# Performance work log

Measured on AMD Instinct MI355X. Metric: run time of the kernel, lower is better.

The kernel has to match this reference:

```python
import jax, jax.numpy as jnp
import numpy as np

V = 9488  # vocab_size + 1
H = 512   # rnn_size = att_hid_size = input_encoding_size
F = 2048  # fc/att feat size

def setup_inputs() -> dict:
    key = jax.random.key(0)
    ks = jax.random.split(key, 16)
    s = 0.02
    return {
        'fc_feats': jax.random.normal(ks[0], (64, F), jnp.float32),
        'att_feats': jax.random.normal(ks[1], (64, 196, F), jnp.float32),
        'seq': jax.random.randint(ks[2], (64, 17), 0, 9487),
        'lin_W': jax.random.normal(ks[3], (H, F), jnp.float32) * s,
        'lin_b': jnp.zeros((H,), jnp.float32),
        'emb': jax.random.uniform(ks[4], (V, H), jnp.float32, -0.1, 0.1),
        'Wih': jax.random.normal(ks[5], (4 * H, H + F), jnp.float32) * s,
        'Whh': jax.random.normal(ks[6], (4 * H, H), jnp.float32) * s,
        'ctx_W': jax.random.normal(ks[7], (H, F), jnp.float32) * s,
        'ctx_b': jnp.zeros((H,), jnp.float32),
        'h2a_W': jax.random.normal(ks[8], (H, H), jnp.float32) * s,
        'h2a_b': jnp.zeros((H,), jnp.float32),
        'alpha_W': jax.random.normal(ks[9], (1, H), jnp.float32) * s,
        'alpha_b': jnp.zeros((1,), jnp.float32),
        'logit_W': jax.random.uniform(ks[10], (V, H), jnp.float32, -0.1, 0.1),
        'logit_b': jnp.zeros((V,), jnp.float32),
    }

def reference(fc_feats, att_feats, seq, lin_W, lin_b, emb, Wih, Whh,
              ctx_W, ctx_b, h2a_W, h2a_b, alpha_W, alpha_b, logit_W, logit_b):
    # init_hidden: h0 = c0 = Linear(fc_feats)  -> [B, H]
    h0 = fc_feats @ lin_W.T + lin_b
    # ctx2att(att_feats) is constant across timesteps -> compute once. [B, L, H]
    p_att = jnp.einsum('blf,hf->blh', att_feats, ctx_W) + ctx_b
    tokens = seq[:, :-1].T  # [T-1, B]

    def step(carry, it):
        h, c = carry
        xt = emb[it]                                   # [B, H]
        att_h = h @ h2a_W.T + h2a_b                    # [B, H]
        dot = jnp.tanh(p_att + att_h[:, None, :])      # [B, L, H]
        e = jnp.einsum('blh,h->bl', dot, alpha_W[0]) + alpha_b[0]
        w = jax.nn.softmax(e, axis=-1)                 # [B, L]
        att_res = jnp.einsum('bl,blf->bf', w, att_feats)  # [B, F]
        x = jnp.concatenate([xt, att_res], axis=1)     # [B, H+F]
        gates = x @ Wih.T + h @ Whh.T                  # bias=False LSTM
        i_g, f_g, g_g, o_g = jnp.split(gates, 4, axis=1)  # torch order i,f,g,o
        c_n = jax.nn.sigmoid(f_g) * c + jax.nn.sigmoid(i_g) * jnp.tanh(g_g)
        h_n = jax.nn.sigmoid(o_g) * jnp.tanh(c_n)
        logp = jax.nn.log_softmax(h_n @ logit_W.T + logit_b, axis=-1)
        return (h_n, c_n), logp

    _, outs = jax.lax.scan(step, (h0, h0), tokens)     # [T-1, B, V]
    return jnp.transpose(outs, (1, 0, 2))              # [B, T-1, V]
```

## Files before the change

### kernel.cpp

```cpp
#include <hip/hip_runtime.h>
#include <stdint.h>
#include <stddef.h>

#define BB 64
#define LL 196
#define FF 2048
#define HH 512
#define VV 9488
#define NPAD 9600
#define TT 16
#define KXX 3072
#define MM (BB * LL)

typedef short short8 __attribute__((ext_vector_type(8)));
typedef short short4v __attribute__((ext_vector_type(4)));
typedef float f32x4 __attribute__((ext_vector_type(4)));
typedef unsigned short u16;
typedef unsigned char u8;

typedef __attribute__((address_space(3))) uint32_t lds_u32_t;
typedef __attribute__((address_space(1))) const uint32_t glb_u32_t;

__device__ __forceinline__ u16 f2bf(float f) {
  uint32_t u = __builtin_bit_cast(uint32_t, f);
  u += 0x7FFFu + ((u >> 16) & 1u);
  return (u16)(u >> 16);
}
__device__ __forceinline__ float bf2f(u16 s) {
  return __builtin_bit_cast(float, ((uint32_t)s) << 16);
}
__device__ __forceinline__ float fast_tanh(float x) {
  return 1.0f - 2.0f / (1.0f + __expf(2.0f * x));
}
__device__ __forceinline__ float fast_sig(float x) {
  return 1.0f / (1.0f + __expf(-x));
}
__device__ __forceinline__ float wred_sum(float v) {
#pragma unroll
  for (int o = 32; o; o >>= 1) v += __shfl_xor(v, o, 64);
  return v;
}
__device__ __forceinline__ float wred_max(float v) {
#pragma unroll
  for (int o = 32; o; o >>= 1) v = fmaxf(v, __shfl_xor(v, o, 64));
  return v;
}
__device__ __forceinline__ f32x4 mfma16(short8 a, short8 b, f32x4 c) {
  return __builtin_amdgcn_mfma_f32_16x16x32_bf16(a, b, c, 0, 0, 0);
}
__device__ __forceinline__ short8 ldbf(const u16* p) {
  return *reinterpret_cast<const short8*>(p);
}
__device__ __forceinline__ void gload16(const u16* g, u16* l) {
  __builtin_amdgcn_global_load_lds((glb_u32_t*)g, (lds_u32_t*)l, 16, 0, 0);
}

__global__ __launch_bounds__(256) void k_setup(
    const float* __restrict__ ctx_W, u16* __restrict__ ctxWb,
    const float* __restrict__ lin_W, u16* __restrict__ linWb,
    const float* __restrict__ h2a_W, u16* __restrict__ h2aWb,
    const float* __restrict__ logit_W, u16* __restrict__ lWb,
    const float* __restrict__ fc, u16* __restrict__ fcb,
    const float* __restrict__ attf, u16* __restrict__ attb, u8* __restrict__ att8,
    const float* __restrict__ Wih, const float* __restrict__ Whh, u16* __restrict__ Wc,
    const float* __restrict__ emb, const int* __restrict__ seq, u16* __restrict__ Xemb) {
  int blk = blockIdx.x, t = threadIdx.x;
  if (blk < 32264) {
    const float* s; u16* d; int rel;
    bool isAtt = false;
    if (blk < 1024)      { s = ctx_W;   d = ctxWb; rel = blk; }
    else if (blk < 2048) { s = lin_W;   d = linWb; rel = blk - 1024; }
    else if (blk < 2304) { s = h2a_W;   d = h2aWb; rel = blk - 2048; }
    else if (blk < 7048) { s = logit_W; d = lWb;   rel = blk - 2304; }
    else if (blk < 7176) { s = fc;      d = fcb;   rel = blk - 7048; }
    else                 { s = attf;    d = attb;  rel = blk - 7176; isAtt = true; }
    int i = rel * 256 + t;
    float4 v = reinterpret_cast<const float4*>(s)[i];
    ushort4 o; o.x = f2bf(v.x); o.y = f2bf(v.y); o.z = f2bf(v.z); o.w = f2bf(v.w);
    reinterpret_cast<ushort4*>(d)[i] = o;
    if (isAtt && att8) {
      uint32_t p8 = __builtin_amdgcn_cvt_pk_fp8_f32(v.x, v.y, 0u, false);
      p8 = __builtin_amdgcn_cvt_pk_fp8_f32(v.z, v.w, p8, true);
      reinterpret_cast<uint32_t*>(att8)[i] = p8;
    }
  } else if (blk < 38408) {
    int i = (blk - 32264) * 256 + t;
    int idx = i * 4;
    int n = idx / KXX, k = idx - n * KXX;
    const float* p = (k < 2560) ? (Wih + (size_t)n * 2560 + k) : (Whh + (size_t)n * HH + (k - 2560));
    float4 v = *reinterpret_cast<const float4*>(p);
    ushort4 o; o.x = f2bf(v.x); o.y = f2bf(v.y); o.z = f2bf(v.z); o.w = f2bf(v.w);
    reinterpret_cast<ushort4*>(Wc)[i] = o;
  } else {
    int i = (blk - 38408) * 256 + t;
    int idx = i * 4;
    int tt = idx / (BB * HH);
    int r = idx - tt * (BB * HH);
    int b = r / HH, k = r - b * HH;
    int tok = seq[b * 17 + tt];
    float4 v = *reinterpret_cast<const float4*>(emb + (size_t)tok * HH + k);
    ushort4 o; o.x = f2bf(v.x); o.y = f2bf(v.y); o.z = f2bf(v.z); o.w = f2bf(v.w);
    reinterpret_cast<ushort4*>(Xemb)[i] = o;
  }
}

__device__ __forceinline__ void dev_h0(int nt, const u16* __restrict__ fcb, const u16* __restrict__ linWb,
                                       const float* __restrict__ lin_b,
                                       u16* __restrict__ hb, float* __restrict__ c) {
  int lane = threadIdx.x & 63;
  int m0 = (threadIdx.x >> 6) * 16, n0 = nt * 16;
  const u16* xr = fcb + (size_t)(m0 + (lane & 15)) * FF + ((lane >> 4) * 8);
  const u16* wr = linWb + (size_t)(n0 + (lane & 15)) * FF + ((lane >> 4) * 8);
  f32x4 acc = {0.f, 0.f, 0.f, 0.f};
#pragma unroll 8
  for (int kk = 0; kk < 64; ++kk)
    acc = mfma16(ldbf(xr + kk * 32), ldbf(wr + kk * 32), acc);
  int col = n0 + (lane & 15);
  float bias = lin_b[col];
#pragma unroll
  for (int j = 0; j < 4; ++j) {
    int row = m0 + (lane >> 4) * 4 + j;
    float v = acc[j] + bias;
    hb[row * HH + col] = f2bf(v);
    c[row * HH + col] = v;
  }
}

__global__ __launch_bounds__(512) void k_patt(const u16* __restrict__ attb,
                                              const u16* __restrict__ ctxWb, const float* __restrict__ ctx_b,
                                              u16* __restrict__ p_att,
                                              const u16* __restrict__ fcb, const u16* __restrict__ linWb,
                                              const float* __restrict__ lin_b,
                                              u16* __restrict__ hb0, float* __restrict__ c) {
  __shared__ __align__(16) u16 As[128][32];
  __shared__ __align__(16) u16 Bs[128][32];
  int d = blockIdx.x;
  if (d >= 392) {
    if (threadIdx.x < 256) dev_h0(d - 392, fcb, linWb, lin_b, hb0, c);
    return;
  }
  int bid = (d & 7) * 49 + (d >> 3);
  int mb = bid >> 2, nb = bid & 3;
  int m0 = mb * 128, n0 = nb * 128;
  int tid = threadIdx.x;
  int wid = tid >> 6, lane = tid & 63;
  int wr2 = wid >> 2, wc2 = wid & 3;
  int ar = lane & 15, ak = (lane >> 4) * 8;
  const u16* ga = attb + (size_t)(m0 + (tid >> 2)) * FF + (tid & 3) * 8;
  const u16* gb = ctxWb + (size_t)(n0 + (tid >> 2)) * FF + (tid & 3) * 8;
  u16* la = &As[0][0] + tid * 8;
  u16* lb = &Bs[0][0] + tid * 8;

  f32x4 zero = {0.f, 0.f, 0.f, 0.f};
  f32x4 acc[4][2];
#pragma unroll
  for (int i = 0; i < 4; ++i)
#pragma unroll
    for (int j = 0; j < 2; ++j) acc[i][j] = zero;

  for (int ks = 0; ks < 64; ++ks) {
    int k0 = ks * 32;
    __syncthreads();
    gload16(ga + k0, la);
    gload16(gb + k0, lb);
    __syncthreads();
    short8 af[4], bfr[2];
#pragma unroll
    for (int i = 0; i < 4; ++i)
      af[i] = *reinterpret_cast<const short8*>(&As[wr2 * 64 + i * 16 + ar][ak]);
#pragma unroll
    for (int j = 0; j < 2; ++j)
      bfr[j] = *reinterpret_cast<const short8*>(&Bs[wc2 * 32 + j * 16 + ar][ak]);
#pragma unroll
    for (int i = 0; i < 4; ++i)
#pragma unroll
      for (int j = 0; j < 2; ++j)
        acc[i][j] = mfma16(af[i], bfr[j], acc[i][j]);
  }
#pragma unroll
  for (int j = 0; j < 2; ++j) {
    int col = n0 + wc2 * 32 + j * 16 + ar;
    float bias = ctx_b[col];
#pragma unroll
    for (int i = 0; i < 4; ++i)
#pragma unroll
      for (int q = 0; q < 4; ++q) {
        int row = m0 + wr2 * 64 + i * 16 + (lane >> 4) * 4 + q;
        p_att[(size_t)row * HH + col] = f2bf(acc[i][j][q] + bias);
      }
  }
}

__device__ __forceinline__ void dev_atth(int nt, const u16* __restrict__ hb, const u16* __restrict__ h2aWb,
                                         const float* __restrict__ h2ab, float* __restrict__ ah) {
  int lane = threadIdx.x & 63;
  int m0 = (threadIdx.x >> 6) * 16, n0 = nt * 16;
  int ak = (lane >> 4) * 8;
  const u16* xr = hb + (size_t)(m0 + (lane & 15)) * HH + ak;
  const u16* wr = h2aWb + (size_t)(n0 + (lane & 15)) * HH + ak;
  f32x4 acc = {0.f, 0.f, 0.f, 0.f};
#pragma unroll
  for (int kk = 0; kk < 16; ++kk)
    acc = mfma16(ldbf(xr + kk * 32), ldbf(wr + kk * 32), acc);
  int col = n0 + (lane & 15);
  float bias = h2ab[col];
#pragma unroll
  for (int j = 0; j < 4; ++j)
    ah[(size_t)(m0 + (lane >> 4) * 4 + j) * HH + col] = acc[j] + bias;
}

__device__ __forceinline__ void dev_e(int bid4, const u16* __restrict__ p_att, const float* __restrict__ ah,
                                      const float* __restrict__ alphaW, const float* __restrict__ alphab,
                                      float* __restrict__ e) {
  int gw = bid4 * 4 + (threadIdx.x >> 6);
  int lane = threadIdx.x & 63;
  int b = gw / LL, l = gw - b * LL;
  short8 pa = ldbf(p_att + (size_t)gw * HH + lane * 8);
  const float4* ap = reinterpret_cast<const float4*>(ah + (size_t)b * HH + lane * 8);
  float4 a0 = ap[0], a1 = ap[1];
  const float4* wp = reinterpret_cast<const float4*>(alphaW + lane * 8);
  float4 w0 = wp[0], w1 = wp[1];
  float s = fast_tanh(bf2f((u16)pa[0]) + a0.x) * w0.x
          + fast_tanh(bf2f((u16)pa[1]) + a0.y) * w0.y
          + fast_tanh(bf2f((u16)pa[2]) + a0.z) * w0.z
          + fast_tanh(bf2f((u16)pa[3]) + a0.w) * w0.w
          + fast_tanh(bf2f((u16)pa[4]) + a1.x) * w1.x
          + fast_tanh(bf2f((u16)pa[5]) + a1.y) * w1.y
          + fast_tanh(bf2f((u16)pa[6]) + a1.z) * w1.z
          + fast_tanh(bf2f((u16)pa[7]) + a1.w) * w1.w;
  s = wred_sum(s);
  if (!lane) e[b * 256 + l] = s + alphab[0];
}

__global__ __launch_bounds__(256) void k_atth(const u16* __restrict__ hb, const u16* __restrict__ h2aWb,
                                              const float* __restrict__ h2ab, float* __restrict__ ah) {
  dev_atth(blockIdx.x, hb, h2aWb, h2ab, ah);
}
__global__ __launch_bounds__(256) void k_e(const u16* __restrict__ p_att, const float* __restrict__ ah,
                                           const float* __restrict__ alphaW, const float* __restrict__ alphab,
                                           float* __restrict__ e) {
  dev_e(blockIdx.x, p_att, ah, alphaW, alphab, e);
}

template<bool FP8>
__global__ __launch_bounds__(256) void k_attR(const float* __restrict__ e, const u16* __restrict__ attb,
                                              const u8* __restrict__ att8, u16* __restrict__ xatt) {
  __shared__ float w_s[LL];
  __shared__ float red[8];
  __shared__ float part[4][256];
  int b = blockIdx.x >> 3, f8 = blockIdx.x & 7;
  int t = threadIdx.x, wid = t >> 6, lane = t & 63;
  float ev = (t < LL) ? e[b * 256 + t] : -1e30f;
  float m = wred_max(ev);
  if (!lane) red[wid] = m;
  __syncthreads();
  m = fmaxf(fmaxf(red[0], red[1]), fmaxf(red[2], red[3]));
  float ex = __expf(ev - m);
  float s = wred_sum(ex);
  if (!lane) red[4 + wid] = s;
  __syncthreads();
  s = red[4] + red[5] + red[6] + red[7];
  if (t < LL) w_s[t] = ex / s;
  __syncthreads();

  int f0 = f8 * 256 + lane * 4;
  float a0 = 0.f, a1 = 0.f, a2 = 0.f, a3 = 0.f;
  int l0 = wid * 49;
  if (FP8) {
    const u8* ap = att8 + ((size_t)(b * LL + l0)) * FF + f0;
#pragma unroll 7
    for (int l = 0; l < 49; ++l) {
      float wv = w_s[l0 + l];
      uint32_t pv = *reinterpret_cast<const uint32_t*>(ap);
      ap += FF;
      a0 += wv * __builtin_amdgcn_cvt_f32_fp8(pv, 0);
      a1 += wv * __builtin_amdgcn_cvt_f32_fp8(pv, 1);
      a2 += wv * __builtin_amdgcn_cvt_f32_fp8(pv, 2);
      a3 += wv * __builtin_amdgcn_cvt_f32_fp8(pv, 3);
    }
  } else {
    const u16* ap = attb + ((size_t)(b * LL + l0)) * FF + f0;
#pragma unroll 7
    for (int l = 0; l < 49; ++l) {
      float wv = w_s[l0 + l];
      short4v av = *reinterpret_cast<const short4v*>(ap);
      ap += FF;
      a0 += wv * bf2f((u16)av[0]); a1 += wv * bf2f((u16)av[1]);
      a2 += wv * bf2f((u16)av[2]); a3 += wv * bf2f((u16)av[3]);
    }
  }
  *reinterpret_cast<float4*>(&part[wid][lane * 4]) = make_float4(a0, a1, a2, a3);
  __syncthreads();
  float v = part[0][t] + part[1][t] + part[2][t] + part[3][t];
  xatt[(size_t)b * FF + f8 * 256 + t] = f2bf(v);
}

__global__ __launch_bounds__(256) void k_gatelstm(const u16* __restrict__ Xemb, const u16* __restrict__ xatt,
                                                  const u16* __restrict__ hb_in, const u16* __restrict__ Wc,
                                                  float* __restrict__ c, u16* __restrict__ hb_out, int tstep) {
  __shared__ float sm[4][4][16][16];
  int d = blockIdx.x;
  int bid = (d & 7) * 16 + (d >> 3);
  int jt = bid >> 2, mq = bid & 3;
  int m0 = mq * 16;
  int lane = threadIdx.x & 63, kq = threadIdx.x >> 6;
  int ar = lane & 15, ak8 = (lane >> 4) * 8;
  int m = m0 + ar;
  int wn = jt * 16 + ar;
  f32x4 zero = {0.f, 0.f, 0.f, 0.f};
  f32x4 acc[4] = {zero, zero, zero, zero};
  const u16* xr0 = Xemb + ((size_t)tstep * BB + m) * HH;
  const u16* xr1 = xatt + (size_t)m * FF;
  const u16* xr2 = hb_in + (size_t)m * HH;

#pragma unroll 4
  for (int kk = 0; kk < 24; ++kk) {
    int k = kq * 768 + kk * 32 + ak8;
    short8 a;
    if (k < 512)       a = ldbf(xr0 + k);
    else if (k < 2560) a = ldbf(xr1 + (k - 512));
    else               a = ldbf(xr2 + (k - 2560));
    short8 bv[4];
#pragma unroll
    for (int g = 0; g < 4; ++g)
      bv[g] = ldbf(Wc + (size_t)(g * 512 + wn) * KXX + k);
#pragma unroll
    for (int g = 0; g < 4; ++g) acc[g] = mfma16(a, bv[g], acc[g]);
  }
#pragma unroll
  for (int g = 0; g < 4; ++g)
#pragma unroll
    for (int q = 0; q < 4; ++q)
      sm[kq][g][(lane >> 4) * 4 + q][ar] = acc[g][q];
  __syncthreads();
  int r = threadIdx.x >> 4, cc = threadIdx.x & 15;
  float gi = sm[0][0][r][cc] + sm[1][0][r][cc] + sm[2][0][r][cc] + sm[3][0][r][cc];
  float gf = sm[0][1][r][cc] + sm[1][1][r][cc] + sm[2][1][r][cc] + sm[3][1][r][cc];
  float gg = sm[0][2][r][cc] + sm[1][2][r][cc] + sm[2][2][r][cc] + sm[3][2][r][cc];
  float go = sm[0][3][r][cc] + sm[1][3][r][cc] + sm[2][3][r][cc] + sm[3][3][r][cc];
  int idx = (m0 + r) * HH + jt * 16 + cc;
  float cn = fast_sig(gf) * c[idx] + fast_sig(gi) * fast_tanh(gg);
  float hn = fast_sig(go) * fast_tanh(cn);
  c[idx] = cn;
  hb_out[idx] = f2bf(hn);
}

__global__ __launch_bounds__(256) void k_logall(const u16* __restrict__ XhL, const u16* __restrict__ lWb,
                                                const float* __restrict__ lb, float* __restrict__ out) {
  __shared__ __align__(16) u16 As[128][32];
  __shared__ __align__(16) u16 Bs[128][32];
  int d = blockIdx.x;
  int mb = d & 7, nb = d >> 3;
  int m0 = mb * 128, n0 = nb * 128;
  int tid = threadIdx.x;
  int wid = tid >> 6, lane = tid & 63;
  int wr = wid >> 1, wc = wid & 1;
  int ar = lane & 15, ak = (lane >> 4) * 8;
  int rt = tid >> 1, st = tid & 1;
  const u16* agp = XhL + (size_t)(m0 + rt) * HH + st * 16;
  const u16* bgp = lWb + (size_t)(n0 + rt) * HH + st * 16;

  f32x4 zero = {0.f, 0.f, 0.f, 0.f};
  f32x4 acc[4][4];
#pragma unroll
  for (int i = 0; i < 4; ++i)
#pragma unroll
    for (int j = 0; j < 4; ++j) acc[i][j] = zero;

  for (int ks = 0; ks < 16; ++ks) {
    int k0 = ks * 32;
    short8 a0 = ldbf(agp + k0);
    short8 a1 = ldbf(agp + k0 + 8);
    short8 b0 = ldbf(bgp + k0);
    short8 b1 = ldbf(bgp + k0 + 8);
    __syncthreads();
    *reinterpret_cast<short8*>(&As[rt][st * 16]) = a0;
    *reinterpret_cast<short8*>(&As[rt][st * 16 + 8]) = a1;
    *reinterpret_cast<short8*>(&Bs[rt][st * 16]) = b0;
    *reinterpret_cast<short8*>(&Bs[rt][st * 16 + 8]) = b1;
    __syncthreads();
    short8 af[4], bfr[4];
#pragma unroll
    for (int i = 0; i < 4; ++i)
      af[i] = *reinterpret_cast<const short8*>(&As[wr * 64 + i * 16 + ar][ak]);
#pragma unroll
    for (int j = 0; j < 4; ++j)
      bfr[j] = *reinterpret_cast<const short8*>(&Bs[wc * 64 + j * 16 + ar][ak]);
#pragma unroll
    for (int i = 0; i < 4; ++i)
#pragma unroll
      for (int j = 0; j < 4; ++j)
        acc[i][j] = mfma16(af[i], bfr[j], acc[i][j]);
  }
#pragma unroll
  for (int j = 0; j < 4; ++j) {
    int col = n0 + wc * 64 + j * 16 + ar;
    if (col >= VV) continue;
    float bias = lb[col];
#pragma unroll
    for (int i = 0; i < 4; ++i)
#pragma unroll
      for (int q = 0; q < 4; ++q) {
        int row = m0 + wr * 64 + i * 16 + (lane >> 4) * 4 + q;
        int bb = row & 63, ts = row >> 6;
        out[((size_t)(bb * TT + ts)) * VV + col] = acc[i][j][q] + bias;
      }
  }
}

__global__ __launch_bounds__(256) void k_lsmall(float* __restrict__ out) {
  __shared__ float red[8];
  float* row = out + (size_t)blockIdx.x * VV;
  float4* row4 = reinterpret_cast<float4*>(row);
  int t = threadIdx.x, wid = t >> 6, lane = t & 63;
  float4 v[10];
  float m = -1e30f;
#pragma unroll
  for (int p = 0; p < 10; ++p) {
    int i4 = p * 256 + t;
    if (i4 < VV / 4) {
      v[p] = row4[i4];
      m = fmaxf(m, fmaxf(fmaxf(v[p].x, v[p].y), fmaxf(v[p].z, v[p].w)));
    } else {
      v[p] = make_float4(-1e30f, -1e30f, -1e30f, -1e30f);
    }
  }
  m = wred_max(m);
  if (!lane) red[wid] = m;
  __syncthreads();
  m = fmaxf(fmaxf(red[0], red[1]), fmaxf(red[2], red[3]));
  float s = 0.f;
#pragma unroll
  for (int p = 0; p < 10; ++p)
    s += __expf(v[p].x - m) + __expf(v[p].y - m) + __expf(v[p].z - m) + __expf(v[p].w - m);
  s = wred_sum(s);
  if (!lane) red[4 + wid] = s;
  __syncthreads();
  s = red[4] + red[5] + red[6] + red[7];
  float lse = m + __logf(s);
#pragma unroll
  for (int p = 0; p < 10; ++p) {
    int i4 = p * 256 + t;
    if (i4 < VV / 4)
      row4[i4] = make_float4(v[p].x - lse, v[p].y - lse, v[p].z - lse, v[p].w - lse);
  }
}

extern "C" void kernel_launch(void* const* d_in, const int* in_sizes, int n_in,
                              void* d_out, int out_size, void* d_ws, size_t ws_size,
                              hipStream_t stream) {
  const float* fc      = (const float*)d_in[0];
  const float* attf    = (const float*)d_in[1];
  const int*   seq     = (const int*)d_in[2];
  const float* lin_W   = (const float*)d_in[3];
  const float* lin_b   = (const float*)d_in[4];
  const float* emb     = (const float*)d_in[5];
  const float* Wih     = (const float*)d_in[6];
  const float* Whh     = (const float*)d_in[7];
  const float* ctx_W   = (const float*)d_in[8];
  const float* ctx_b   = (const float*)d_in[9];
  const float* h2a_W   = (const float*)d_in[10];
  const float* h2a_b   = (const float*)d_in[11];
  const float* alpha_W = (const float*)d_in[12];
  const float* alpha_b = (const float*)d_in[13];
  const float* logit_W = (const float*)d_in[14];
  const float* logit_b = (const float*)d_in[15];
  float* out = (float*)d_out;

  char* base = (char*)d_ws;
  size_t off = 0;
  auto alloc = [&](size_t bytes) -> char* {
    off = (off + 255) & ~(size_t)255;
    char* p = base + off;
    off += bytes;
    return p;
  };
  u16*   p_att  = (u16*)alloc((size_t)MM * HH * 2);
  u16*   ctxWb  = (u16*)alloc((size_t)HH * FF * 2);
  u16*   linWb  = (u16*)alloc((size_t)HH * FF * 2);
  u16*   fcb    = (u16*)alloc((size_t)BB * FF * 2);
  u16*   h2aWb  = (u16*)alloc((size_t)HH * HH * 2);
  u16*   Xemb   = (u16*)alloc((size_t)TT * BB * HH * 2);
  float* c      = (float*)alloc((size_t)BB * HH * 4);
  u16*   Xh     = (u16*)alloc((size_t)(TT + 1) * BB * HH * 2);
  u16*   xatt   = (u16*)alloc((size_t)BB * FF * 2);
  float* eb     = (float*)alloc((size_t)BB * 256 * 4);
  float* ah     = (float*)alloc((size_t)BB * HH * 4);
  u16*   Wc     = (u16*)alloc((size_t)2048 * KXX * 2);
  u16*   lWb    = (u16*)alloc((size_t)NPAD * HH * 2);
  u16*   attb   = (u16*)alloc((size_t)MM * FF * 2);
  bool useF8 = (((off + 255) & ~(size_t)255) + (size_t)MM * FF) <= ws_size;
  u8* att8 = useF8 ? (u8*)alloc((size_t)MM * FF) : nullptr;

  k_setup<<<38920, 256, 0, stream>>>(ctx_W, ctxWb, lin_W, linWb, h2a_W, h2aWb, logit_W, lWb,
                                     fc, fcb, attf, attb, att8, Wih, Whh, Wc, emb, seq, Xemb);
  k_patt<<<424, 512, 0, stream>>>(attb, ctxWb, ctx_b, p_att, fcb, linWb, lin_b, Xh, c);

  k_atth<<<32, 256, 0, stream>>>(Xh, h2aWb, h2a_b, ah);
  k_e<<<MM / 4, 256, 0, stream>>>(p_att, ah, alpha_W, alpha_b, eb);

  for (int t = 0; t < TT; ++t) {
    u16* ht  = Xh + (size_t)t * BB * HH;
    u16* htn = Xh + (size_t)(t + 1) * BB * HH;
    if (useF8) k_attR<true><<<512, 256, 0, stream>>>(eb, attb, att8, xatt);
    else       k_attR<false><<<512, 256, 0, stream>>>(eb, attb, att8, xatt);
    k_gatelstm<<<128, 256, 0, stream>>>(Xemb, xatt, ht, Wc, c, htn, t);
    if (t < TT - 1) {
      k_atth<<<32, 256, 0, stream>>>(htn, h2aWb, h2a_b, ah);
      k_e<<<MM / 4, 256, 0, stream>>>(p_att, ah, alpha_W, alpha_b, eb);
    }
  }
  k_logall<<<600, 256, 0, stream>>>(Xh + (size_t)BB * HH, lWb, logit_b, out);
  k_lsmall<<<TT * BB, 256, 0, stream>>>(out);
}
```

Before: 705.8 us.

## Move attention projection and p_att storage to FP8, drop bf16 att copy

```diff
diff --git a/kernel.cpp b/kernel.cpp
--- a/kernel.cpp
+++ b/kernel.cpp
@@ -17,6 +17,7 @@
 typedef float f32x4 __attribute__((ext_vector_type(4)));
 typedef unsigned short u16;
 typedef unsigned char u8;
+typedef unsigned long long u64;
 
 typedef __attribute__((address_space(3))) uint32_t lds_u32_t;
 typedef __attribute__((address_space(1))) const uint32_t glb_u32_t;
@@ -48,41 +49,51 @@
 __device__ __forceinline__ f32x4 mfma16(short8 a, short8 b, f32x4 c) {
   return __builtin_amdgcn_mfma_f32_16x16x32_bf16(a, b, c, 0, 0, 0);
 }
+__device__ __forceinline__ f32x4 mfma8(u64 a, u64 b, f32x4 c) {
+  return __builtin_amdgcn_mfma_f32_16x16x32_fp8_fp8((long long)a, (long long)b, c, 0, 0, 0);
+}
 __device__ __forceinline__ short8 ldbf(const u16* p) {
   return *reinterpret_cast<const short8*>(p);
 }
-__device__ __forceinline__ void gload16(const u16* g, u16* l) {
+__device__ __forceinline__ u8 f2fp8(float v) {
+  return (u8)(__builtin_amdgcn_cvt_pk_fp8_f32(v, v, 0u, false) & 0xFFu);
+}
+__device__ __forceinline__ void gload16(const void* g, void* l) {
   __builtin_amdgcn_global_load_lds((glb_u32_t*)g, (lds_u32_t*)l, 16, 0, 0);
 }
 
 __global__ __launch_bounds__(256) void k_setup(
-    const float* __restrict__ ctx_W, u16* __restrict__ ctxWb,
+    const float* __restrict__ ctx_W, u8* __restrict__ ctxW8,
     const float* __restrict__ lin_W, u16* __restrict__ linWb,
     const float* __restrict__ h2a_W, u16* __restrict__ h2aWb,
     const float* __restrict__ logit_W, u16* __restrict__ lWb,
     const float* __restrict__ fc, u16* __restrict__ fcb,
-    const float* __restrict__ attf, u16* __restrict__ attb, u8* __restrict__ att8,
+    const float* __restrict__ attf, u8* __restrict__ att8,
     const float* __restrict__ Wih, const float* __restrict__ Whh, u16* __restrict__ Wc,
     const float* __restrict__ emb, const int* __restrict__ seq, u16* __restrict__ Xemb) {
   int blk = blockIdx.x, t = threadIdx.x;
-  if (blk < 32264) {
+  if (blk < 1024) {
+    int i = blk * 256 + t;
+    float4 v = reinterpret_cast<const float4*>(ctx_W)[i];
+    uint32_t p8 = __builtin_amdgcn_cvt_pk_fp8_f32(v.x, v.y, 0u, false);
+    p8 = __builtin_amdgcn_cvt_pk_fp8_f32(v.z, v.w, p8, true);
+    reinterpret_cast<uint32_t*>(ctxW8)[i] = p8;
+  } else if (blk < 7176) {
     const float* s; u16* d; int rel;
-    bool isAtt = false;
-    if (blk < 1024)      { s = ctx_W;   d = ctxWb; rel = blk; }
-    else if (blk < 2048) { s = lin_W;   d = linWb; rel = blk - 1024; }
+    if (blk < 2048)      { s = lin_W;   d = linWb; rel = blk - 1024; }
     else if (blk < 2304) { s = h2a_W;   d = h2aWb; rel = blk - 2048; }
     else if (blk < 7048) { s = logit_W; d = lWb;   rel = blk - 2304; }
-    else if (blk < 7176) { s = fc;      d = fcb;   rel = blk - 7048; }
-    else                 { s = attf;    d = attb;  rel = blk - 7176; isAtt = true; }
+    else                 { s = fc;      d = fcb;   rel = blk - 7048; }
     int i = rel * 256 + t;
     float4 v = reinterpret_cast<const float4*>(s)[i];
     ushort4 o; o.x = f2bf(v.x); o.y = f2bf(v.y); o.z = f2bf(v.z); o.w = f2bf(v.w);
     reinterpret_cast<ushort4*>(d)[i] = o;
-    if (isAtt && att8) {
-      uint32_t p8 = __builtin_amdgcn_cvt_pk_fp8_f32(v.x, v.y, 0u, false);
-      p8 = __builtin_amdgcn_cvt_pk_fp8_f32(v.z, v.w, p8, true);
-      reinterpret_cast<uint32_t*>(att8)[i] = p8;
-    }
+  } else if (blk < 32264) {
+    int i = (blk - 7176) * 256 + t;
+    float4 v = reinterpret_cast<const float4*>(attf)[i];
+    uint32_t p8 = __builtin_amdgcn_cvt_pk_fp8_f32(v.x, v.y, 0u, false);
+    p8 = __builtin_amdgcn_cvt_pk_fp8_f32(v.z, v.w, p8, true);
+    reinterpret_cast<uint32_t*>(att8)[i] = p8;
   } else if (blk < 38408) {
     int i = (blk - 32264) * 256 + t;
     int idx = i * 4;
@@ -126,14 +137,14 @@
   }
 }
 
-__global__ __launch_bounds__(512) void k_patt(const u16* __restrict__ attb,
-                                              const u16* __restrict__ ctxWb, const float* __restrict__ ctx_b,
-                                              u16* __restrict__ p_att,
+__global__ __launch_bounds__(512) void k_patt(const u8* __restrict__ att8,
+                                              const u8* __restrict__ ctxW8, const float* __restrict__ ctx_b,
+                                              u8* __restrict__ p_att8,
                                               const u16* __restrict__ fcb, const u16* __restrict__ linWb,
                                               const float* __restrict__ lin_b,
                                               u16* __restrict__ hb0, float* __restrict__ c) {
-  __shared__ __align__(16) u16 As[128][32];
-  __shared__ __align__(16) u16 Bs[128][32];
+  __shared__ __align__(16) u8 As[128][32];
+  __shared__ __align__(16) u8 Bs[128][32];
   int d = blockIdx.x;
   if (d >= 392) {
     if (threadIdx.x < 256) dev_h0(d - 392, fcb, linWb, lin_b, hb0, c);
@@ -145,11 +156,13 @@
   int tid = threadIdx.x;
   int wid = tid >> 6, lane = tid & 63;
   int wr2 = wid >> 2, wc2 = wid & 3;
-  int ar = lane & 15, ak = (lane >> 4) * 8;
-  const u16* ga = attb + (size_t)(m0 + (tid >> 2)) * FF + (tid & 3) * 8;
-  const u16* gb = ctxWb + (size_t)(n0 + (tid >> 2)) * FF + (tid & 3) * 8;
-  u16* la = &As[0][0] + tid * 8;
-  u16* lb = &Bs[0][0] + tid * 8;
+  int ar = lane & 15;
+  int akb = (lane >> 4) * 8;
+  bool isA = tid < 256;
+  int t2 = tid & 255;
+  const u8* gsrc = isA ? (att8 + (size_t)(m0 + (t2 >> 1)) * FF + (t2 & 1) * 16)
+                       : (ctxW8 + (size_t)(n0 + (t2 >> 1)) * FF + (t2 & 1) * 16);
+  u8* ldst = isA ? (&As[0][0] + t2 * 16) : (&Bs[0][0] + t2 * 16);
 
   f32x4 zero = {0.f, 0.f, 0.f, 0.f};
   f32x4 acc[4][2];
@@ -161,21 +174,20 @@
   for (int ks = 0; ks < 64; ++ks) {
     int k0 = ks * 32;
     __syncthreads();
-    gload16(ga + k0, la);
-    gload16(gb + k0, lb);
+    gload16(gsrc + k0, ldst);
     __syncthreads();
-    short8 af[4], bfr[2];
+    u64 af[4], bfr[2];
 #pragma unroll
     for (int i = 0; i < 4; ++i)
-      af[i] = *reinterpret_cast<const short8*>(&As[wr2 * 64 + i * 16 + ar][ak]);
+      af[i] = *reinterpret_cast<const u64*>(&As[wr2 * 64 + i * 16 + ar][akb]);
 #pragma unroll
     for (int j = 0; j < 2; ++j)
-      bfr[j] = *reinterpret_cast<const short8*>(&Bs[wc2 * 32 + j * 16 + ar][ak]);
+      bfr[j] = *reinterpret_cast<const u64*>(&Bs[wc2 * 32 + j * 16 + ar][akb]);
 #pragma unroll
     for (int i = 0; i < 4; ++i)
 #pragma unroll
       for (int j = 0; j < 2; ++j)
-        acc[i][j] = mfma16(af[i], bfr[j], acc[i][j]);
+        acc[i][j] = mfma8(af[i], bfr[j], acc[i][j]);
   }
 #pragma unroll
   for (int j = 0; j < 2; ++j) {
@@ -186,7 +198,7 @@
 #pragma unroll
       for (int q = 0; q < 4; ++q) {
         int row = m0 + wr2 * 64 + i * 16 + (lane >> 4) * 4 + q;
-        p_att[(size_t)row * HH + col] = f2bf(acc[i][j][q] + bias);
+        p_att8[(size_t)row * HH + col] = f2fp8(acc[i][j][q] + bias);
       }
   }
 }
@@ -209,25 +221,34 @@
     ah[(size_t)(m0 + (lane >> 4) * 4 + j) * HH + col] = acc[j] + bias;
 }
 
-__device__ __forceinline__ void dev_e(int bid4, const u16* __restrict__ p_att, const float* __restrict__ ah,
+__device__ __forceinline__ void dev_e(int bid4, const u8* __restrict__ p_att8, const float* __restrict__ ah,
                                       const float* __restrict__ alphaW, const float* __restrict__ alphab,
                                       float* __restrict__ e) {
   int gw = bid4 * 4 + (threadIdx.x >> 6);
   int lane = threadIdx.x & 63;
   int b = gw / LL, l = gw - b * LL;
-  short8 pa = ldbf(p_att + (size_t)gw * HH + lane * 8);
+  u64 pv = *reinterpret_cast<const u64*>(p_att8 + (size_t)gw * HH + lane * 8);
+  uint32_t lo = (uint32_t)pv, hi = (uint32_t)(pv >> 32);
+  float p0 = __builtin_amdgcn_cvt_f32_fp8(lo, 0);
+  float p1 = __builtin_amdgcn_cvt_f32_fp8(lo, 1);
+  float p2 = __builtin_amdgcn_cvt_f32_fp8(lo, 2);
+  float p3 = __builtin_amdgcn_cvt_f32_fp8(lo, 3);
+  float p4 = __builtin_amdgcn_cvt_f32_fp8(hi, 0);
+  float p5 = __builtin_amdgcn_cvt_f32_fp8(hi, 1);
+  float p6 = __builtin_amdgcn_cvt_f32_fp8(hi, 2);
+  float p7 = __builtin_amdgcn_cvt_f32_fp8(hi, 3);
   const float4* ap = reinterpret_cast<const float4*>(ah + (size_t)b * HH + lane * 8);
   float4 a0 = ap[0], a1 = ap[1];
   const float4* wp = reinterpret_cast<const float4*>(alphaW + lane * 8);
   float4 w0 = wp[0], w1 = wp[1];
-  float s = fast_tanh(bf2f((u16)pa[0]) + a0.x) * w0.x
-          + fast_tanh(bf2f((u16)pa[1]) + a0.y) * w0.y
-          + fast_tanh(bf2f((u16)pa[2]) + a0.z) * w0.z
-          + fast_tanh(bf2f((u16)pa[3]) + a0.w) * w0.w
-          + fast_tanh(bf2f((u16)pa[4]) + a1.x) * w1.x
-          + fast_tanh(bf2f((u16)pa[5]) + a1.y) * w1.y
-          + fast_tanh(bf2f((u16)pa[6]) + a1.z) * w1.z
-          + fast_tanh(bf2f((u16)pa[7]) + a1.w) * w1.w;
+  float s = fast_tanh(p0 + a0.x) * w0.x
+          + fast_tanh(p1 + a0.y) * w0.y
+          + fast_tanh(p2 + a0.z) * w0.z
+          + fast_tanh(p3 + a0.w) * w0.w
+          + fast_tanh(p4 + a1.x) * w1.x
+          + fast_tanh(p5 + a1.y) * w1.y
+          + fast_tanh(p6 + a1.z) * w1.z
+          + fast_tanh(p7 + a1.w) * w1.w;
   s = wred_sum(s);
   if (!lane) e[b * 256 + l] = s + alphab[0];
 }
@@ -236,15 +257,14 @@
                                               const float* __restrict__ h2ab, float* __restrict__ ah) {
   dev_atth(blockIdx.x, hb, h2aWb, h2ab, ah);
 }
-__global__ __launch_bounds__(256) void k_e(const u16* __restrict__ p_att, const float* __restrict__ ah,
+__global__ __launch_bounds__(256) void k_e(const u8* __restrict__ p_att8, const float* __restrict__ ah,
                                            const float* __restrict__ alphaW, const float* __restrict__ alphab,
                                            float* __restrict__ e) {
-  dev_e(blockIdx.x, p_att, ah, alphaW, alphab, e);
-}
-
-template<bool FP8>
-__global__ __launch_bounds__(256) void k_attR(const float* __restrict__ e, const u16* __restrict__ attb,
-                                              const u8* __restrict__ att8, u16* __restrict__ xatt) {
+  dev_e(blockIdx.x, p_att8, ah, alphaW, alphab, e);
+}
+
+__global__ __launch_bounds__(256) void k_attR(const float* __restrict__ e, const u8* __restrict__ att8,
+                                              u16* __restrict__ xatt) {
   __shared__ float w_s[LL];
   __shared__ float red[8];
   __shared__ float part[4][256];
@@ -266,28 +286,16 @@
   int f0 = f8 * 256 + lane * 4;
   float a0 = 0.f, a1 = 0.f, a2 = 0.f, a3 = 0.f;
   int l0 = wid * 49;
-  if (FP8) {
-    const u8* ap = att8 + ((size_t)(b * LL + l0)) * FF + f0;
+  const u8* ap = att8 + ((size_t)(b * LL + l0)) * FF + f0;
 #pragma unroll 7
-    for (int l = 0; l < 49; ++l) {
-      float wv = w_s[l0 + l];
-      uint32_t pv = *reinterpret_cast<const uint32_t*>(ap);
-      ap += FF;
-      a0 += wv * __builtin_amdgcn_cvt_f32_fp8(pv, 0);
-      a1 += wv * __builtin_amdgcn_cvt_f32_fp8(pv, 1);
-      a2 += wv * __builtin_amdgcn_cvt_f32_fp8(pv, 2);
-      a3 += wv * __builtin_amdgcn_cvt_f32_fp8(pv, 3);
-    }
-  } else {
-    const u16* ap = attb + ((size_t)(b * LL + l0)) * FF + f0;
-#pragma unroll 7
-    for (int l = 0; l < 49; ++l) {
-      float wv = w_s[l0 + l];
-      short4v av = *reinterpret_cast<const short4v*>(ap);
-      ap += FF;
-      a0 += wv * bf2f((u16)av[0]); a1 += wv * bf2f((u16)av[1]);
-      a2 += wv * bf2f((u16)av[2]); a3 += wv * bf2f((u16)av[3]);
-    }
+  for (int l = 0; l < 49; ++l) {
+    float wv = w_s[l0 + l];
+    uint32_t pv = *reinterpret_cast<const uint32_t*>(ap);
+    ap += FF;
+    a0 += wv * __builtin_amdgcn_cvt_f32_fp8(pv, 0);
+    a1 += wv * __builtin_amdgcn_cvt_f32_fp8(pv, 1);
+    a2 += wv * __builtin_amdgcn_cvt_f32_fp8(pv, 2);
+    a3 += wv * __builtin_amdgcn_cvt_f32_fp8(pv, 3);
   }
   *reinterpret_cast<float4*>(&part[wid][lane * 4]) = make_float4(a0, a1, a2, a3);
   __syncthreads();
@@ -475,8 +483,8 @@
     off += bytes;
     return p;
   };
-  u16*   p_att  = (u16*)alloc((size_t)MM * HH * 2);
-  u16*   ctxWb  = (u16*)alloc((size_t)HH * FF * 2);
+  u8*    p_att8 = (u8*)alloc((size_t)MM * HH);
+  u8*    ctxW8  = (u8*)alloc((size_t)HH * FF);
   u16*   linWb  = (u16*)alloc((size_t)HH * FF * 2);
   u16*   fcb    = (u16*)alloc((size_t)BB * FF * 2);
   u16*   h2aWb  = (u16*)alloc((size_t)HH * HH * 2);
@@ -488,26 +496,24 @@
   float* ah     = (float*)alloc((size_t)BB * HH * 4);
   u16*   Wc     = (u16*)alloc((size_t)2048 * KXX * 2);
   u16*   lWb    = (u16*)alloc((size_t)NPAD * HH * 2);
-  u16*   attb   = (u16*)alloc((size_t)MM * FF * 2);
-  bool useF8 = (((off + 255) & ~(size_t)255) + (size_t)MM * FF) <= ws_size;
-  u8* att8 = useF8 ? (u8*)alloc((size_t)MM * FF) : nullptr;
-
-  k_setup<<<38920, 256, 0, stream>>>(ctx_W, ctxWb, lin_W, linWb, h2a_W, h2aWb, logit_W, lWb,
-                                     fc, fcb, attf, attb, att8, Wih, Whh, Wc, emb, seq, Xemb);
-  k_patt<<<424, 512, 0, stream>>>(attb, ctxWb, ctx_b, p_att, fcb, linWb, lin_b, Xh, c);
+  u8*    att8   = (u8*)alloc((size_t)MM * FF);
+  (void)ws_size;
+
+  k_setup<<<38920, 256, 0, stream>>>(ctx_W, ctxW8, lin_W, linWb, h2a_W, h2aWb, logit_W, lWb,
+                                     fc, fcb, attf, att8, Wih, Whh, Wc, emb, seq, Xemb);
+  k_patt<<<424, 512, 0, stream>>>(att8, ctxW8, ctx_b, p_att8, fcb, linWb, lin_b, Xh, c);
 
   k_atth<<<32, 256, 0, stream>>>(Xh, h2aWb, h2a_b, ah);
-  k_e<<<MM / 4, 256, 0, stream>>>(p_att, ah, alpha_W, alpha_b, eb);
+  k_e<<<MM / 4, 256, 0, stream>>>(p_att8, ah, alpha_W, alpha_b, eb);
 
   for (int t = 0; t < TT; ++t) {
     u16* ht  = Xh + (size_t)t * BB * HH;
     u16* htn = Xh + (size_t)(t + 1) * BB * HH;
-    if (useF8) k_attR<true><<<512, 256, 0, stream>>>(eb, attb, att8, xatt);
-    else       k_attR<false><<<512, 256, 0, stream>>>(eb, attb, att8, xatt);
+    k_attR<<<512, 256, 0, stream>>>(eb, att8, xatt);
     k_gatelstm<<<128, 256, 0, stream>>>(Xemb, xatt, ht, Wc, c, htn, t);
     if (t < TT - 1) {
       k_atth<<<32, 256, 0, stream>>>(htn, h2aWb, h2a_b, ah);
-      k_e<<<MM / 4, 256, 0, stream>>>(p_att, ah, alpha_W, alpha_b, eb);
+      k_e<<<MM / 4, 256, 0, stream>>>(p_att8, ah, alpha_W, alpha_b, eb);
     }
   }
   k_logall<<<600, 256, 0, stream>>>(Xh + (size_t)BB * HH, lWb, logit_b, out);
```

Result: no change. 700.6 us (-0.7%).
